# Kernel optimization log

Measured on AMD Instinct MI355X. Metric: run time of the kernel, lower is better.

## Reference

```python
import jax, jax.numpy as jnp
import numpy as np

B = 4096      # batch of stimuli
U = 4096      # max_nunits
D = 16        # n_dims


def setup_inputs() -> dict:
    key = jax.random.key(0)
    k1, k2, k3 = jax.random.split(key, 3)
    # forward arg: stimuli, shaped [B, 1, D] so they broadcast against the U unit batch dim
    inp = jax.random.normal(k1, (B, 1, D), dtype=jnp.float32)
    # learned params (torch inits units to zeros; use small randn so outputs are nontrivial)
    units = 0.5 * jax.random.normal(k2, (U, D), dtype=jnp.float32)
    # attn param is [U, D, D]; module forces it diagonal each call. Build diagonal with
    # positive per-dim scales (torch init would be sqrt(0.02) * I per unit).
    diag = jax.random.uniform(k3, (U, D), dtype=jnp.float32, minval=0.05, maxval=0.3)
    attn = jax.vmap(jnp.diag)(diag)  # [U, D, D]
    return {"input": inp, "units": units, "attn": attn}


def reference(input, units, attn):
    # diag of scale_tril = per-dim std dev, clamped like torch.clamp(min=1e-6)
    diag = jnp.clip(jnp.diagonal(attn, axis1=-2, axis2=-1), 1e-6)  # [U, D]
    # MVN with scale_tril = diag(s): logpdf = -0.5*sum(((x-mu)/s)^2) - sum(log s) - 0.5*D*log(2pi)
    z = (input - units) / diag                       # [B, U, D] via broadcasting
    half_log_2pi = 0.5 * jnp.float32(np.log(2.0 * np.pi))
    log_prob = (-0.5 * jnp.sum(z * z, axis=-1)       # [B, U]
                - jnp.sum(jnp.log(diag), axis=-1)    # [U]
                - jnp.float32(D) * half_log_2pi)
    return jnp.exp(log_prob)                         # activations, [B, U]
```

## Files before the change

kernel.cpp:

```cpp
#include <hip/hip_runtime.h>
#include <hip/hip_bf16.h>
#include <math.h>


#define TPB 256
#define DD  16
#define UB  32
#define BB  256

typedef float v2f __attribute__((ext_vector_type(2)));

static constexpr float L2E   = 1.4426950408889634f;
static constexpr float HL2PI = 0.91893853320467274f;

__global__ __launch_bounds__(TPB, 5) void mva_tile(
    const float* __restrict__ x,
    const float* __restrict__ units,
    const float* __restrict__ attn,
    float* __restrict__ out,
    int U)
{
    const int tid    = threadIdx.x;
    const int u_base = blockIdx.x * UB;
    const int b_base = blockIdx.y * BB;

    __shared__ float xs[BB][DD];
    __shared__ float a1L[DD][UB + 2];
    __shared__ float a2L[DD][UB + 2];
    __shared__ float biasL[UB];

    const float* xb = x + (size_t)b_base * DD;
#pragma unroll
    for (int r = 0; r < (BB * DD) / (TPB * 4); ++r) {
        const int q = (r * TPB + tid) * 4;
        *reinterpret_cast<float4*>(&xs[0][0] + q) =
            *reinterpret_cast<const float4*>(xb + q);
    }

    {
        const int ul = tid >> 3;
        const int d0 = (tid & 7) * 2;
        const int u  = u_base + ul;
        float2 m = *reinterpret_cast<const float2*>(units + (size_t)u * DD + d0);
        const float* ar = attn + (size_t)u * DD * DD;
        float s0 = fmaxf(ar[d0 * (DD + 1)], 1e-6f);
        float s1 = fmaxf(ar[(d0 + 1) * (DD + 1)], 1e-6f);
        float w0 = 1.f / (s0 * s0);
        float w1 = 1.f / (s1 * s1);
        a1L[d0][ul]     = L2E * m.x * w0;
        a2L[d0][ul]     = -0.5f * L2E * w0;
        a1L[d0 + 1][ul] = L2E * m.y * w1;
        a2L[d0 + 1][ul] = -0.5f * L2E * w1;
        float bn = -0.5f * (m.x * m.x * w0 + m.y * m.y * w1)
                 - (logf(s0) + logf(s1));
        bn += __shfl_xor(bn, 1, 8);
        bn += __shfl_xor(bn, 2, 8);
        bn += __shfl_xor(bn, 4, 8);
        if ((tid & 7) == 0) biasL[ul] = L2E * (bn - DD * HL2PI);
    }
    __syncthreads();

    const int up = tid & 15;
    const int br = tid >> 4;
    v2f a1p[DD], a2p[DD];
#pragma unroll
    for (int d = 0; d < DD; ++d) {
        a1p[d] = *reinterpret_cast<const v2f*>(&a1L[d][up * 2]);
        a2p[d] = *reinterpret_cast<const v2f*>(&a2L[d][up * 2]);
    }
    const v2f biasp = *reinterpret_cast<const v2f*>(&biasL[up * 2]);

    float* orow = out + (size_t)b_base * U + u_base + up * 2;
#pragma unroll 2
    for (int it = 0; it < BB / 16; ++it) {
        const int b = it * 16 + br;
        v2f acc = biasp;
#pragma unroll
        for (int j = 0; j < 4; ++j) {
            float4 xv = *reinterpret_cast<const float4*>(&xs[b][4 * j]);
            const int d = 4 * j;
            v2f xx, t;
            xx = (v2f){xv.x, xv.x};
            t   = __builtin_elementwise_fma(xx, a2p[d + 0], a1p[d + 0]);
            acc = __builtin_elementwise_fma(xx, t, acc);
            xx = (v2f){xv.y, xv.y};
            t   = __builtin_elementwise_fma(xx, a2p[d + 1], a1p[d + 1]);
            acc = __builtin_elementwise_fma(xx, t, acc);
            xx = (v2f){xv.z, xv.z};
            t   = __builtin_elementwise_fma(xx, a2p[d + 2], a1p[d + 2]);
            acc = __builtin_elementwise_fma(xx, t, acc);
            xx = (v2f){xv.w, xv.w};
            t   = __builtin_elementwise_fma(xx, a2p[d + 3], a1p[d + 3]);
            acc = __builtin_elementwise_fma(xx, t, acc);
        }
        float2 o;
        o.x = __builtin_amdgcn_exp2f(acc[0]);
        o.y = __builtin_amdgcn_exp2f(acc[1]);
        *reinterpret_cast<float2*>(orow + (size_t)b * U) = o;
    }
}

extern "C" void kernel_launch(void* const* d_in, const int* in_sizes, int n_in,
                              void* d_out, int out_size, void* d_ws, size_t ws_size,
                              hipStream_t stream) {
    const float* x     = (const float*)d_in[0];
    const float* units = (const float*)d_in[1];
    const float* attn  = (const float*)d_in[2];
    float* out = (float*)d_out;

    const int B = in_sizes[0] / DD;
    const int U = in_sizes[1] / DD;

    dim3 grid(U / UB, B / BB);
    mva_tile<<<grid, TPB, 0, stream>>>(x, units, attn, out, U);
}
```

Measured before the change: 23.07 us.

## Use persistent double-buffered x staging with 4-unit-per-thread float4 output

Each block now covers 2048 batch rows in four phases of 512, double-buffering the x tile in padded shared memory so the next phase loads while the current one computes. Per-unit coefficients are computed once per block, which amortises that setup across more rows. Each thread now handles 4 units and writes float4 stores. Register pressure rises and the grid shrinks to 128x2 blocks of 512 threads, which may underfill the GPU.

New measurement: 24.11 us. +4.5%, slower.

```diff
diff --git a/kernel.cpp b/kernel.cpp
--- a/kernel.cpp
+++ b/kernel.cpp
@@ -3,17 +3,19 @@
 #include <math.h>
 
 
-#define TPB 256
-#define DD  16
-#define UB  32
-#define BB  256
+#define TPB  512
+#define DD   16
+#define UB   32
+#define BCH  512
+#define NPH  4
+#define XST  (DD + 4)
 
 typedef float v2f __attribute__((ext_vector_type(2)));
 
 static constexpr float L2E   = 1.4426950408889634f;
 static constexpr float HL2PI = 0.91893853320467274f;
 
-__global__ __launch_bounds__(TPB, 5) void mva_tile(
+__global__ __launch_bounds__(TPB, 2) void mva_big(
     const float* __restrict__ x,
     const float* __restrict__ units,
     const float* __restrict__ attn,
@@ -22,81 +24,102 @@
 {
     const int tid    = threadIdx.x;
     const int u_base = blockIdx.x * UB;
-    const int b_base = blockIdx.y * BB;
+    const int b_base = blockIdx.y * (BCH * NPH);
 
-    __shared__ float xs[BB][DD];
-    __shared__ float a1L[DD][UB + 2];
-    __shared__ float a2L[DD][UB + 2];
-    __shared__ float biasL[UB];
+    __shared__ __align__(16) float xs[2][BCH][XST];
+    __shared__ __align__(16) float a1L[DD][UB + 4];
+    __shared__ __align__(16) float a2L[DD][UB + 4];
+    __shared__ __align__(16) float biasL[UB];
 
-    const float* xb = x + (size_t)b_base * DD;
-#pragma unroll
-    for (int r = 0; r < (BB * DD) / (TPB * 4); ++r) {
-        const int q = (r * TPB + tid) * 4;
-        *reinterpret_cast<float4*>(&xs[0][0] + q) =
-            *reinterpret_cast<const float4*>(xb + q);
+    {
+        const int ul = tid >> 4, d = tid & 15;
+        const int u  = u_base + ul;
+        float s  = fmaxf(attn[(size_t)u * DD * DD + d * (DD + 1)], 1e-6f);
+        float w  = 1.f / (s * s);
+        float mu = units[u * DD + d];
+        a1L[d][ul] = L2E * mu * w;
+        a2L[d][ul] = -0.5f * L2E * w;
+        float bn = -0.5f * mu * mu * w - logf(s);
+        bn += __shfl_xor(bn, 1, 16);
+        bn += __shfl_xor(bn, 2, 16);
+        bn += __shfl_xor(bn, 4, 16);
+        bn += __shfl_xor(bn, 8, 16);
+        if (d == 0) biasL[ul] = L2E * (bn - DD * HL2PI);
     }
 
-    {
-        const int ul = tid >> 3;
-        const int d0 = (tid & 7) * 2;
-        const int u  = u_base + ul;
-        float2 m = *reinterpret_cast<const float2*>(units + (size_t)u * DD + d0);
-        const float* ar = attn + (size_t)u * DD * DD;
-        float s0 = fmaxf(ar[d0 * (DD + 1)], 1e-6f);
-        float s1 = fmaxf(ar[(d0 + 1) * (DD + 1)], 1e-6f);
-        float w0 = 1.f / (s0 * s0);
-        float w1 = 1.f / (s1 * s1);
-        a1L[d0][ul]     = L2E * m.x * w0;
-        a2L[d0][ul]     = -0.5f * L2E * w0;
-        a1L[d0 + 1][ul] = L2E * m.y * w1;
-        a2L[d0 + 1][ul] = -0.5f * L2E * w1;
-        float bn = -0.5f * (m.x * m.x * w0 + m.y * m.y * w1)
-                 - (logf(s0) + logf(s1));
-        bn += __shfl_xor(bn, 1, 8);
-        bn += __shfl_xor(bn, 2, 8);
-        bn += __shfl_xor(bn, 4, 8);
-        if ((tid & 7) == 0) biasL[ul] = L2E * (bn - DD * HL2PI);
-    }
+    auto stage = [&](int ph) {
+        const float* xb = x + (size_t)(b_base + ph * BCH) * DD;
+        float* dst = &xs[ph & 1][0][0];
+#pragma unroll
+        for (int r = 0; r < (BCH * DD) / (TPB * 4); ++r) {
+            const int q   = (r * TPB + tid) * 4;
+            const int row = q >> 4, col = q & 15;
+            *reinterpret_cast<float4*>(dst + row * XST + col) =
+                *reinterpret_cast<const float4*>(xb + q);
+        }
+    };
+
+    stage(0);
     __syncthreads();
 
-    const int up = tid & 15;
-    const int br = tid >> 4;
-    v2f a1p[DD], a2p[DD];
+    const int uq = tid & 7;
+    const int br = tid >> 3;
+    v2f a1A[DD], a1B[DD], a2A[DD], a2B[DD];
 #pragma unroll
     for (int d = 0; d < DD; ++d) {
-        a1p[d] = *reinterpret_cast<const v2f*>(&a1L[d][up * 2]);
-        a2p[d] = *reinterpret_cast<const v2f*>(&a2L[d][up * 2]);
+        float4 q1 = *reinterpret_cast<const float4*>(&a1L[d][uq * 4]);
+        a1A[d] = (v2f){q1.x, q1.y};  a1B[d] = (v2f){q1.z, q1.w};
+        float4 q2 = *reinterpret_cast<const float4*>(&a2L[d][uq * 4]);
+        a2A[d] = (v2f){q2.x, q2.y};  a2B[d] = (v2f){q2.z, q2.w};
     }
-    const v2f biasp = *reinterpret_cast<const v2f*>(&biasL[up * 2]);
+    float4 bq = *reinterpret_cast<const float4*>(&biasL[uq * 4]);
+    const v2f biasA = (v2f){bq.x, bq.y}, biasB = (v2f){bq.z, bq.w};
 
-    float* orow = out + (size_t)b_base * U + u_base + up * 2;
+#pragma unroll 1
+    for (int ph = 0; ph < NPH; ++ph) {
+        if (ph + 1 < NPH) stage(ph + 1);
+        const float* xp = &xs[ph & 1][0][0];
+        float* ob = out + (size_t)(b_base + ph * BCH) * U + u_base + uq * 4;
+
 #pragma unroll 2
-    for (int it = 0; it < BB / 16; ++it) {
-        const int b = it * 16 + br;
-        v2f acc = biasp;
+        for (int it = 0; it < BCH / 64; ++it) {
+            const int b = it * 64 + br;
+            const float* xr = xp + b * XST;
+            v2f accA = biasA, accB = biasB;
 #pragma unroll
-        for (int j = 0; j < 4; ++j) {
-            float4 xv = *reinterpret_cast<const float4*>(&xs[b][4 * j]);
-            const int d = 4 * j;
-            v2f xx, t;
-            xx = (v2f){xv.x, xv.x};
-            t   = __builtin_elementwise_fma(xx, a2p[d + 0], a1p[d + 0]);
-            acc = __builtin_elementwise_fma(xx, t, acc);
-            xx = (v2f){xv.y, xv.y};
-            t   = __builtin_elementwise_fma(xx, a2p[d + 1], a1p[d + 1]);
-            acc = __builtin_elementwise_fma(xx, t, acc);
-            xx = (v2f){xv.z, xv.z};
-            t   = __builtin_elementwise_fma(xx, a2p[d + 2], a1p[d + 2]);
-            acc = __builtin_elementwise_fma(xx, t, acc);
-            xx = (v2f){xv.w, xv.w};
-            t   = __builtin_elementwise_fma(xx, a2p[d + 3], a1p[d + 3]);
-            acc = __builtin_elementwise_fma(xx, t, acc);
+            for (int j = 0; j < 4; ++j) {
+                float4 xv = *reinterpret_cast<const float4*>(xr + 4 * j);
+                const int d = 4 * j;
+                v2f xx, t;
+                xx = (v2f){xv.x, xv.x};
+                t = __builtin_elementwise_fma(xx, a2A[d + 0], a1A[d + 0]);
+                accA = __builtin_elementwise_fma(xx, t, accA);
+                t = __builtin_elementwise_fma(xx, a2B[d + 0], a1B[d + 0]);
+                accB = __builtin_elementwise_fma(xx, t, accB);
+                xx = (v2f){xv.y, xv.y};
+                t = __builtin_elementwise_fma(xx, a2A[d + 1], a1A[d + 1]);
+                accA = __builtin_elementwise_fma(xx, t, accA);
+                t = __builtin_elementwise_fma(xx, a2B[d + 1], a1B[d + 1]);
+                accB = __builtin_elementwise_fma(xx, t, accB);
+                xx = (v2f){xv.z, xv.z};
+                t = __builtin_elementwise_fma(xx, a2A[d + 2], a1A[d + 2]);
+                accA = __builtin_elementwise_fma(xx, t, accA);
+                t = __builtin_elementwise_fma(xx, a2B[d + 2], a1B[d + 2]);
+                accB = __builtin_elementwise_fma(xx, t, accB);
+                xx = (v2f){xv.w, xv.w};
+                t = __builtin_elementwise_fma(xx, a2A[d + 3], a1A[d + 3]);
+                accA = __builtin_elementwise_fma(xx, t, accA);
+                t = __builtin_elementwise_fma(xx, a2B[d + 3], a1B[d + 3]);
+                accB = __builtin_elementwise_fma(xx, t, accB);
+            }
+            float4 o;
+            o.x = __builtin_amdgcn_exp2f(accA[0]);
+            o.y = __builtin_amdgcn_exp2f(accA[1]);
+            o.z = __builtin_amdgcn_exp2f(accB[0]);
+            o.w = __builtin_amdgcn_exp2f(accB[1]);
+            *reinterpret_cast<float4*>(ob + (size_t)b * U) = o;
         }
-        float2 o;
-        o.x = __builtin_amdgcn_exp2f(acc[0]);
-        o.y = __builtin_amdgcn_exp2f(acc[1]);
-        *reinterpret_cast<float2*>(orow + (size_t)b * U) = o;
+        __syncthreads();
     }
 }
 
@@ -111,6 +134,6 @@
     const int B = in_sizes[0] / DD;
     const int U = in_sizes[1] / DD;
 
-    dim3 grid(U / UB, B / BB);
-    mva_tile<<<grid, TPB, 0, stream>>>(x, units, attn, out, U);
+    dim3 grid(U / UB, B / (BCH * NPH));
+    mva_big<<<grid, TPB, 0, stream>>>(x, units, attn, out, U);
 }
```
